# Kernel optimization log

Hardware: AMD Instinct MI355X
Metric: run time of the kernel (lower is better)

## Reference

```python
import jax, jax.numpy as jnp
import numpy as np

B, S, D, H = 2, 2048, 1024, 16
HD = D // H  # head_dim = 64
LN_EPS = 1e-5


def setup_inputs() -> dict:
    key = jax.random.key(0)
    ks = jax.random.split(key, 14)
    w = 0.02  # weight init scale
    return {
        "q": jax.random.normal(ks[0], (B, S, D), jnp.float32),
        "k": jax.random.normal(ks[1], (B, S, D), jnp.float32),
        "v": jax.random.normal(ks[2], (B, S, D), jnp.float32),
        "mask": jnp.zeros((B, 1, S, S), dtype=bool),
        "training": 0,
        "wq_w": jax.random.normal(ks[3], (D, D), jnp.float32) * w,
        "wq_b": jnp.zeros((D,), jnp.float32),
        "wk_w": jax.random.normal(ks[4], (D, D), jnp.float32) * w,
        "wk_b": jnp.zeros((D,), jnp.float32),
        "wv_w": jax.random.normal(ks[5], (D, D), jnp.float32) * w,
        "wv_b": jnp.zeros((D,), jnp.float32),
        "wo_w": jax.random.normal(ks[6], (D, D), jnp.float32) * w,
        "wo_b": jnp.zeros((D,), jnp.float32),
        "ln_g": jnp.ones((D,), jnp.float32),
        "ln_b": jnp.zeros((D,), jnp.float32),
    }


def _linear(x, w, b):
    # torch nn.Linear: x @ W.T + b, W is [out, in]
    return jnp.einsum('bsd,od->bso', x, w) + b


def _split_heads(x):
    b, s, _ = x.shape
    return x.reshape(b, s, H, HD).transpose(0, 2, 1, 3)  # [B,H,S,HD]


def reference(q, k, v, mask, training, wq_w, wq_b, wk_w, wk_b, wv_w, wv_b,
              wo_w, wo_b, ln_g, ln_b):
    residual = q
    Q = _split_heads(_linear(q, wq_w, wq_b))
    K = _split_heads(_linear(k, wk_w, wk_b))
    V = _split_heads(_linear(v, wv_w, wv_b))
    # source computes sqrt(dk) in float16, then adds 1e-8
    dk = jnp.sqrt(jnp.asarray(HD, jnp.float16)).astype(jnp.float32) + 1e-8
    score = jnp.einsum('bhqd,bhkd->bhqk', Q, K) / dk  # [B,H,S,S]
    # NOTE: source applies NO softmax; masked score is used directly.
    attn = jnp.where(mask, -jnp.inf, score)
    ctx = jnp.einsum('bhqk,bhkd->bhqd', attn, V)  # [B,H,S,HD]
    b, _, s, _ = ctx.shape
    ctx = ctx.transpose(0, 2, 1, 3).reshape(b, s, D)  # [B,S,D]
    o = _linear(ctx, wo_w, wo_b)
    # dropout is identity in eval mode
    x = residual + o
    mu = jnp.mean(x, axis=-1, keepdims=True)
    var = jnp.mean(jnp.square(x - mu), axis=-1, keepdims=True)
    return ln_g * (x - mu) * jax.lax.rsqrt(var + LN_EPS) + ln_b
```

## Files before the change

### kernel.cpp

```cpp
#include <hip/hip_runtime.h>


typedef __bf16 bf16;
typedef __bf16 bf16x8 __attribute__((ext_vector_type(8)));
typedef float f32x4 __attribute__((ext_vector_type(4)));

#define MFMA16(a, b, c) __builtin_amdgcn_mfma_f32_16x16x32_bf16(a, b, c, 0, 0, 0)
#define BARRIER() asm volatile("s_barrier" ::: "memory")
#define VMCNT4() asm volatile("s_waitcnt vmcnt(4)" ::: "memory")
#define VMCNT0() asm volatile("s_waitcnt vmcnt(0)" ::: "memory")
#define LGKM0()                                        \
  do {                                                 \
    asm volatile("s_waitcnt lgkmcnt(0)" ::: "memory"); \
    __builtin_amdgcn_sched_barrier(0);                 \
  } while (0)

__device__ __forceinline__ bf16x8 ld8(const bf16* p) { return *(const bf16x8*)p; }

__device__ __forceinline__ void gload16(const void* g, void* l) {
  __builtin_amdgcn_global_load_lds((__attribute__((address_space(1))) void*)(g),
                                   (__attribute__((address_space(3))) void*)(l), 16, 0, 0);
}

__device__ __forceinline__ int swz4(int row) { return (row ^ (row >> 2)) & 3; }

__device__ __forceinline__ bf16x8 cvt8(f32x4 lo, f32x4 hi) {
  bf16x8 o;
  o[0] = (bf16)lo[0]; o[1] = (bf16)lo[1]; o[2] = (bf16)lo[2]; o[3] = (bf16)lo[3];
  o[4] = (bf16)hi[0]; o[5] = (bf16)hi[1]; o[6] = (bf16)hi[2]; o[7] = (bf16)hi[3];
  return o;
}

__device__ __forceinline__ void compute16(const char* buf, const int aoff[4], const int boff[4],
                                          f32x4 (&acc)[4][4]) {
  bf16x8 av[4], bv[4];
#pragma unroll
  for (int i = 0; i < 4; i++) av[i] = *(const bf16x8*)(buf + aoff[i]);
#pragma unroll
  for (int j = 0; j < 4; j++) bv[j] = *(const bf16x8*)(buf + boff[j]);
  __builtin_amdgcn_s_setprio(1);
#pragma unroll
  for (int i = 0; i < 4; i++)
#pragma unroll
    for (int j = 0; j < 4; j++) acc[i][j] = MFMA16(av[i], bv[j], acc[i][j]);
  __builtin_amdgcn_s_setprio(0);
}

__device__ __forceinline__ void ring128(const bf16* __restrict__ A, const bf16* __restrict__ B,
                                        char* lds, f32x4 (&acc)[4][4]) {
  const int t = threadIdx.x;
  const int lane = t & 63, wid = t >> 6;
  const int wr = wid >> 1, wc = wid & 1;
  const int r16 = lane & 15, kg = lane >> 4;

  int aoff[4], boff[4];
#pragma unroll
  for (int i = 0; i < 4; i++) {
    int row = wr * 64 + i * 16 + r16;
    aoff[i] = row * 64 + ((kg ^ swz4(row)) << 4);
    row = wc * 64 + i * 16 + r16;
    boff[i] = 8192 + row * 64 + ((kg ^ swz4(row)) << 4);
  }

  const int r1 = t >> 2, c = t & 3, r2 = r1 + 64;
  const bf16* pa1 = A + (size_t)r1 * 1024 + (c ^ swz4(r1)) * 8;
  const bf16* pa2 = A + (size_t)r2 * 1024 + (c ^ swz4(r2)) * 8;
  const bf16* pb1 = B + (size_t)r1 * 1024 + (c ^ swz4(r1)) * 8;
  const bf16* pb2 = B + (size_t)r2 * 1024 + (c ^ swz4(r2)) * 8;
  const int d1 = wid << 10, d2 = 4096 + (wid << 10);

#pragma unroll
  for (int p = 0; p < 2; p++) {
    char* d = lds + p * 16384;
    gload16(pa1 + p * 32, d + d1);
    gload16(pa2 + p * 32, d + d2);
    gload16(pb1 + p * 32, d + 8192 + d1);
    gload16(pb2 + p * 32, d + 8192 + d2);
  }
  pa1 += 64; pa2 += 64; pb1 += 64; pb2 += 64;

  int cb = 0, rb = 2;
  for (int kt = 0; kt < 30; kt++) {
    VMCNT4();
    BARRIER();
    {
      char* d = lds + rb * 16384;
      gload16(pa1, d + d1);
      gload16(pa2, d + d2);
      gload16(pb1, d + 8192 + d1);
      gload16(pb2, d + 8192 + d2);
      pa1 += 32; pa2 += 32; pb1 += 32; pb2 += 32;
    }
    compute16(lds + cb * 16384, aoff, boff, acc);
    LGKM0();
    cb = (cb == 2) ? 0 : cb + 1;
    rb = (rb == 2) ? 0 : rb + 1;
  }
  VMCNT4(); BARRIER();
  compute16(lds + cb * 16384, aoff, boff, acc);
  LGKM0();
  cb = (cb == 2) ? 0 : cb + 1;
  VMCNT0(); BARRIER();
  compute16(lds + cb * 16384, aoff, boff, acc);
}

__device__ __forceinline__ void proj_epi(f32x4 (&acc)[4][4], const float* bias,
                                         bf16* __restrict__ C, int m0, int n0) {
  const int lane = threadIdx.x & 63, wid = threadIdx.x >> 6;
  const int wr = wid >> 1, wc = wid & 1, r16 = lane & 15, kg = lane >> 4;
#pragma unroll
  for (int j = 0; j < 4; j++) {
    const int col = n0 + wc * 64 + j * 16 + r16;
    const float bj = bias[col];
#pragma unroll
    for (int i = 0; i < 4; i++) {
      const int row = m0 + wr * 64 + i * 16 + kg * 4;
#pragma unroll
      for (int r = 0; r < 4; r++)
        C[(size_t)(row + r) * 1024 + col] = (bf16)(acc[i][j][r] + bj);
    }
  }
}

__global__ __launch_bounds__(256) void cvt_q_kernel(
    const float* __restrict__ q, const float* __restrict__ wq,
    bf16* __restrict__ q_bf, bf16* __restrict__ wq_bf, float* __restrict__ Mz) {
  const int bid = blockIdx.x;
  if (bid >= 2560) {
    float* p = Mz + (size_t)(bid - 2560) * 2048 + threadIdx.x * 8;
    *(f32x4*)p = f32x4{0.f, 0.f, 0.f, 0.f};
    *(f32x4*)(p + 4) = f32x4{0.f, 0.f, 0.f, 0.f};
    return;
  }
  const float* s; bf16* d; int x;
  if (bid < 2048) { s = q; d = q_bf; x = bid; }
  else            { s = wq; d = wq_bf; x = bid - 2048; }
  const size_t i = ((size_t)x * 256 + threadIdx.x) * 8;
  *(bf16x8*)(d + i) = cvt8(*(const f32x4*)(s + i), *(const f32x4*)(s + i + 4));
}

__global__ __launch_bounds__(256, 3) void fat1_kernel(
    const bf16* __restrict__ q_bf, const bf16* __restrict__ wq_bf,
    const float* __restrict__ bq, bf16* __restrict__ Q_bf,
    const float* __restrict__ k, const float* __restrict__ v,
    const float* __restrict__ wk, const float* __restrict__ wv,
    bf16* __restrict__ kv_bf, bf16* __restrict__ wkv_bf) {
  __shared__ __align__(1024) char lds[49152];
  const int wg = blockIdx.x;
  if (wg < 256) {
    const int swz = (wg & 7) * 32 + (wg >> 3);
    const int mt = swz >> 3, nt = swz & 7;
    const int m0 = mt * 128, n0 = nt * 128;
    f32x4 acc[4][4] = {};
    ring128(q_bf + (size_t)m0 * 1024, wq_bf + (size_t)n0 * 1024, lds, acc);
    proj_epi(acc, bq, Q_bf, m0, n0);
    return;
  }
  const int idx = wg - 256;
  const float* s; bf16* d; size_t dof; int x;
  if (idx < 4096) {
    const int y = idx >> 11; x = idx & 2047;
    s = (y == 0) ? k : v;
    d = kv_bf; dof = (size_t)y * 4194304u;
  } else {
    const int y = (idx - 4096) >> 9; x = (idx - 4096) & 511;
    s = (y == 0) ? wk : wv;
    d = wkv_bf; dof = (size_t)y * 1048576u;
  }
  const size_t i = ((size_t)x * 256 + threadIdx.x) * 8;
  *(bf16x8*)(d + dof + i) = cvt8(*(const f32x4*)(s + i), *(const f32x4*)(s + i + 4));
}

__global__ __launch_bounds__(256, 3) void gemm_proj_kv(
    const bf16* __restrict__ kv_bf, const bf16* __restrict__ wkv_bf,
    const float* __restrict__ bk, const float* __restrict__ bv,
    bf16* __restrict__ KV_out) {
  __shared__ __align__(1024) char lds[49152];
  const int wg = blockIdx.x;
  const int swz = (wg & 7) * 64 + (wg >> 3);
  const int mt = swz >> 3, nt = swz & 7;
  const int m0 = mt * 128, n0 = nt * 128;
  const int z = mt >> 5;

  f32x4 acc[4][4] = {};
  ring128(kv_bf + (size_t)m0 * 1024, wkv_bf + (size_t)z * 1048576u + (size_t)n0 * 1024, lds, acc);
  proj_epi(acc, z == 0 ? bk : bv, KV_out, m0, n0);
}

__global__ __launch_bounds__(256) void ktv_kernel(
    const bf16* __restrict__ Kb, const bf16* __restrict__ Vb, float* __restrict__ M) {
  const int bh = blockIdx.x >> 3, sc = blockIdx.x & 7;
  const int b = bh >> 4, h = bh & 15;
  __shared__ bf16 Kl[64][136];
  __shared__ bf16 Vl[64][136];
  const int t = threadIdx.x;
  const int l = t & 63, w = t >> 6;
  const int r16 = l & 15, kg = l >> 4;
  f32x4 acc[4] = {};
  for (int sub = 0; sub < 2; ++sub) {
    const int s0 = sc * 256 + sub * 128;
    const size_t base = ((size_t)b * 2048 + s0) * 1024 + h * 64;
    if (sub) __syncthreads();
#pragma unroll
    for (int p = 0; p < 4; p++) {
      const int chunk = p * 256 + t;
      const int s = chunk >> 3, d0 = (chunk & 7) * 8;
      bf16x8 kv = ld8(Kb + base + (size_t)s * 1024 + d0);
      bf16x8 vv = ld8(Vb + base + (size_t)s * 1024 + d0);
#pragma unroll
      for (int e = 0; e < 8; e++) { Kl[d0 + e][s] = kv[e]; Vl[d0 + e][s] = vv[e]; }
    }
    __syncthreads();
#pragma unroll
    for (int ks = 0; ks < 4; ks++) {
      bf16x8 a = ld8(&Kl[w * 16 + r16][ks * 32 + kg * 8]);
#pragma unroll
      for (int j = 0; j < 4; j++) {
        bf16x8 bvv = ld8(&Vl[j * 16 + r16][ks * 32 + kg * 8]);
        acc[j] = MFMA16(a, bvv, acc[j]);
      }
    }
  }
  float* Mh = M + (size_t)bh * 4096;
#pragma unroll
  for (int j = 0; j < 4; j++)
#pragma unroll
    for (int r = 0; r < 4; r++)
      atomicAdd(&Mh[(w * 16 + kg * 4 + r) * 64 + j * 16 + r16], acc[j][r]);
}

__global__ __launch_bounds__(256) void gt_kernel(
    const float* __restrict__ Wo, const float* __restrict__ M, bf16* __restrict__ Gt) {
  const int bid = blockIdx.x;
  const int b = bid >> 7, h = (bid >> 3) & 15, nt = bid & 7;
  const int n0 = nt * 128;
  const float* Mh = M + (size_t)((b << 4) + h) * 4096;
  const int l = threadIdx.x & 63, w = threadIdx.x >> 6;
  const int r16 = l & 15, kg = l >> 4;
  f32x4 acc[2][4] = {};
#pragma unroll
  for (int kk = 0; kk < 2; kk++) {
    bf16x8 a[2];
#pragma unroll
    for (int i = 0; i < 2; i++) {
      const float* wp = Wo + (size_t)(n0 + w * 32 + i * 16 + r16) * 1024 + h * 64 + kk * 32 + kg * 8;
      a[i] = cvt8(*(const f32x4*)wp, *(const f32x4*)(wp + 4));
    }
#pragma unroll
    for (int j = 0; j < 4; j++) {
      const float* mp = Mh + (j * 16 + r16) * 64 + kk * 32 + kg * 8;
      f32x4 m0v = *(const f32x4*)mp;
      f32x4 m1v = *(const f32x4*)(mp + 4);
      f32x4 sl = {m0v[0] * 0.125f, m0v[1] * 0.125f, m0v[2] * 0.125f, m0v[3] * 0.125f};
      f32x4 sh = {m1v[0] * 0.125f, m1v[1] * 0.125f, m1v[2] * 0.125f, m1v[3] * 0.125f};
      bf16x8 bv = cvt8(sl, sh);
#pragma unroll
      for (int i = 0; i < 2; i++) acc[i][j] = MFMA16(a[i], bv, acc[i][j]);
    }
  }
  bf16* G = Gt + (size_t)b * 1048576u;
#pragma unroll
  for (int i = 0; i < 2; i++)
#pragma unroll
    for (int j = 0; j < 4; j++)
#pragma unroll
      for (int r = 0; r < 4; r++)
        G[(size_t)(n0 + w * 32 + i * 16 + kg * 4 + r) * 1024 + h * 64 + j * 16 + r16] =
            (bf16)acc[i][j][r];
}

__global__ __launch_bounds__(256, 3) void gemm_out_r(
    const bf16* __restrict__ Q, const bf16* __restrict__ Gt,
    const float* __restrict__ bo, const float* __restrict__ resid, bf16* __restrict__ xb) {
  __shared__ __align__(1024) char lds[49152];
  const int wg = blockIdx.x;
  const int swz = (wg & 7) * 32 + (wg >> 3);
  const int mt = swz >> 3, nt = swz & 7;
  const int m0 = mt * 128, n0 = nt * 128;

  f32x4 acc[4][4] = {};
  ring128(Q + (size_t)m0 * 1024, Gt + (size_t)(m0 >> 11) * 1048576u + (size_t)n0 * 1024, lds, acc);

  const int lane = threadIdx.x & 63, wid = threadIdx.x >> 6;
  const int wr = wid >> 1, wc = wid & 1, r16 = lane & 15, kg = lane >> 4;
#pragma unroll
  for (int j = 0; j < 4; j++) {
    const int col = n0 + wc * 64 + j * 16 + r16;
    const float bj = bo[col];
#pragma unroll
    for (int i = 0; i < 4; i++) {
      const int row = m0 + wr * 64 + i * 16 + kg * 4;
#pragma unroll
      for (int r = 0; r < 4; r++) {
        const size_t off = (size_t)(row + r) * 1024 + col;
        xb[off] = (bf16)(acc[i][j][r] + bj + resid[off]);
      }
    }
  }
}

__global__ __launch_bounds__(256) void ln_kernel(
    const bf16* __restrict__ xb, const float* __restrict__ g, const float* __restrict__ bb,
    float* __restrict__ out) {
  const int lane = threadIdx.x & 63, wid = threadIdx.x >> 6;
  const int row = (blockIdx.x << 2) + wid;
  const bf16* xr = xb + (size_t)row * 1024;
  bf16x8 h0 = ld8(xr + lane * 16);
  bf16x8 h1 = ld8(xr + lane * 16 + 8);
  float v[16];
#pragma unroll
  for (int e = 0; e < 8; e++) { v[e] = (float)h0[e]; v[8 + e] = (float)h1[e]; }
  float s = 0.f, s2 = 0.f;
#pragma unroll
  for (int e = 0; e < 16; e++) { s += v[e]; s2 += v[e] * v[e]; }
#pragma unroll
  for (int m = 32; m; m >>= 1) { s += __shfl_xor(s, m); s2 += __shfl_xor(s2, m); }
  const float mu = s * (1.0f / 1024.0f);
  const float rstd = rsqrtf(s2 * (1.0f / 1024.0f) - mu * mu + 1e-5f);
  float* orow = out + (size_t)row * 1024 + lane * 16;
#pragma unroll
  for (int e = 0; e < 4; e++) {
    f32x4 gg = *(const f32x4*)(g + lane * 16 + e * 4);
    f32x4 bv = *(const f32x4*)(bb + lane * 16 + e * 4);
    f32x4 o;
#pragma unroll
    for (int u = 0; u < 4; u++) o[u] = gg[u] * ((v[e * 4 + u] - mu) * rstd) + bv[u];
    *(f32x4*)(orow + e * 4) = o;
  }
}

extern "C" void kernel_launch(void* const* d_in, const int* in_sizes, int n_in,
                              void* d_out, int out_size, void* d_ws, size_t ws_size,
                              hipStream_t stream) {
  (void)in_sizes; (void)n_in; (void)out_size; (void)ws_size;
  const float* q    = (const float*)d_in[0];
  const float* k    = (const float*)d_in[1];
  const float* v    = (const float*)d_in[2];
  const float* wq_w = (const float*)d_in[5];
  const float* wq_b = (const float*)d_in[6];
  const float* wk_w = (const float*)d_in[7];
  const float* wk_b = (const float*)d_in[8];
  const float* wv_w = (const float*)d_in[9];
  const float* wv_b = (const float*)d_in[10];
  const float* wo_w = (const float*)d_in[11];
  const float* wo_b = (const float*)d_in[12];
  const float* ln_g = (const float*)d_in[13];
  const float* ln_b = (const float*)d_in[14];
  float* out = (float*)d_out;

  bf16* wsb    = (bf16*)d_ws;
  bf16* q_bf   = wsb;
  bf16* kv_bf  = wsb + 4194304u;
  bf16* w_bf   = wsb + 12582912u;
  bf16* QKV_bf = wsb + 15728640u;
  float* M     = (float*)(wsb + 28311552u);
  bf16* Gt     = wsb;
  bf16* xb     = wsb + 2097152u;

  cvt_q_kernel<<<2624, 256, 0, stream>>>(q, wq_w, q_bf, w_bf, M);
  fat1_kernel<<<5376, 256, 0, stream>>>(q_bf, w_bf, wq_b, QKV_bf,
                                        k, v, wk_w, wv_w, kv_bf, w_bf + 1048576u);
  gemm_proj_kv<<<512, 256, 0, stream>>>(kv_bf, w_bf + 1048576u, wk_b, wv_b,
                                        QKV_bf + 4194304u);
  ktv_kernel<<<256, 256, 0, stream>>>(QKV_bf + 4194304u, QKV_bf + 8388608u, M);
  gt_kernel<<<256, 256, 0, stream>>>(wo_w, M, Gt);
  gemm_out_r<<<256, 256, 0, stream>>>(QKV_bf, Gt, wo_b, q, xb);
  ln_kernel<<<1024, 256, 0, stream>>>(xb, ln_g, ln_b, out);
}
```

Before: 92.05 us.

## Reschedule stages so K/V projection runs first and overlaps Q work

Reorders the pipeline. The K/V/weight conversion now runs first. The K/V projection GEMM runs in the same launch as the Q conversion. The Q projection GEMM shares a launch with the K^T V reduction, which reuses the GEMM's LDS buffer. This drops one kernel launch and lets independent memory-bound and compute-bound work overlap inside fused launches. The risk is load imbalance between the heterogeneous blocks and LDS/occupancy limits imposed on the ktv part by the 48KB allocation.

```diff
diff --git a/kernel.cpp b/kernel.cpp
--- a/kernel.cpp
+++ b/kernel.cpp
@@ -122,29 +122,61 @@
   }
 }
 
-__global__ __launch_bounds__(256) void cvt_q_kernel(
-    const float* __restrict__ q, const float* __restrict__ wq,
-    bf16* __restrict__ q_bf, bf16* __restrict__ wq_bf, float* __restrict__ Mz) {
+__global__ __launch_bounds__(256) void cvt_kvw_kernel(
+    const float* __restrict__ k, const float* __restrict__ v,
+    const float* __restrict__ wk, const float* __restrict__ wv,
+    bf16* __restrict__ kv_bf, bf16* __restrict__ wkv_bf, float* __restrict__ Mz) {
   const int bid = blockIdx.x;
-  if (bid >= 2560) {
-    float* p = Mz + (size_t)(bid - 2560) * 2048 + threadIdx.x * 8;
+  if (bid >= 5120) {
+    float* p = Mz + (size_t)(bid - 5120) * 2048 + threadIdx.x * 8;
     *(f32x4*)p = f32x4{0.f, 0.f, 0.f, 0.f};
     *(f32x4*)(p + 4) = f32x4{0.f, 0.f, 0.f, 0.f};
     return;
   }
+  const float* s; bf16* d; size_t dof; int x;
+  if (bid < 4096) {
+    const int y = bid >> 11; x = bid & 2047;
+    s = (y == 0) ? k : v;
+    d = kv_bf; dof = (size_t)y * 4194304u;
+  } else {
+    const int idx = bid - 4096; const int y = idx >> 9; x = idx & 511;
+    s = (y == 0) ? wk : wv;
+    d = wkv_bf; dof = (size_t)y * 1048576u;
+  }
+  const size_t i = ((size_t)x * 256 + threadIdx.x) * 8;
+  *(bf16x8*)(d + dof + i) = cvt8(*(const f32x4*)(s + i), *(const f32x4*)(s + i + 4));
+}
+
+__global__ __launch_bounds__(256, 3) void fat_a_kernel(
+    const bf16* __restrict__ kv_bf, const bf16* __restrict__ wkv_bf,
+    const float* __restrict__ bk, const float* __restrict__ bv, bf16* __restrict__ KV_out,
+    const float* __restrict__ q, const float* __restrict__ wq,
+    bf16* __restrict__ q_bf, bf16* __restrict__ wq_bf) {
+  __shared__ __align__(1024) char lds[49152];
+  const int wg = blockIdx.x;
+  if (wg < 512) {
+    const int swz = (wg & 7) * 64 + (wg >> 3);
+    const int mt = swz >> 3, nt = swz & 7;
+    const int m0 = mt * 128, n0 = nt * 128;
+    const int z = mt >> 5;
+    f32x4 acc[4][4] = {};
+    ring128(kv_bf + (size_t)m0 * 1024, wkv_bf + (size_t)z * 1048576u + (size_t)n0 * 1024,
+            lds, acc);
+    proj_epi(acc, z == 0 ? bk : bv, KV_out, m0, n0);
+    return;
+  }
+  const int idx = wg - 512;
   const float* s; bf16* d; int x;
-  if (bid < 2048) { s = q; d = q_bf; x = bid; }
-  else            { s = wq; d = wq_bf; x = bid - 2048; }
+  if (idx < 2048) { s = q; d = q_bf; x = idx; }
+  else            { s = wq; d = wq_bf; x = idx - 2048; }
   const size_t i = ((size_t)x * 256 + threadIdx.x) * 8;
   *(bf16x8*)(d + i) = cvt8(*(const f32x4*)(s + i), *(const f32x4*)(s + i + 4));
 }
 
-__global__ __launch_bounds__(256, 3) void fat1_kernel(
+__global__ __launch_bounds__(256, 3) void fat_b_kernel(
     const bf16* __restrict__ q_bf, const bf16* __restrict__ wq_bf,
     const float* __restrict__ bq, bf16* __restrict__ Q_bf,
-    const float* __restrict__ k, const float* __restrict__ v,
-    const float* __restrict__ wk, const float* __restrict__ wv,
-    bf16* __restrict__ kv_bf, bf16* __restrict__ wkv_bf) {
+    const bf16* __restrict__ Kb, const bf16* __restrict__ Vb, float* __restrict__ M) {
   __shared__ __align__(1024) char lds[49152];
   const int wg = blockIdx.x;
   if (wg < 256) {
@@ -156,43 +188,11 @@
     proj_epi(acc, bq, Q_bf, m0, n0);
     return;
   }
-  const int idx = wg - 256;
-  const float* s; bf16* d; size_t dof; int x;
-  if (idx < 4096) {
-    const int y = idx >> 11; x = idx & 2047;
-    s = (y == 0) ? k : v;
-    d = kv_bf; dof = (size_t)y * 4194304u;
-  } else {
-    const int y = (idx - 4096) >> 9; x = (idx - 4096) & 511;
-    s = (y == 0) ? wk : wv;
-    d = wkv_bf; dof = (size_t)y * 1048576u;
-  }
-  const size_t i = ((size_t)x * 256 + threadIdx.x) * 8;
-  *(bf16x8*)(d + dof + i) = cvt8(*(const f32x4*)(s + i), *(const f32x4*)(s + i + 4));
-}
-
-__global__ __launch_bounds__(256, 3) void gemm_proj_kv(
-    const bf16* __restrict__ kv_bf, const bf16* __restrict__ wkv_bf,
-    const float* __restrict__ bk, const float* __restrict__ bv,
-    bf16* __restrict__ KV_out) {
-  __shared__ __align__(1024) char lds[49152];
-  const int wg = blockIdx.x;
-  const int swz = (wg & 7) * 64 + (wg >> 3);
-  const int mt = swz >> 3, nt = swz & 7;
-  const int m0 = mt * 128, n0 = nt * 128;
-  const int z = mt >> 5;
-
-  f32x4 acc[4][4] = {};
-  ring128(kv_bf + (size_t)m0 * 1024, wkv_bf + (size_t)z * 1048576u + (size_t)n0 * 1024, lds, acc);
-  proj_epi(acc, z == 0 ? bk : bv, KV_out, m0, n0);
-}
-
-__global__ __launch_bounds__(256) void ktv_kernel(
-    const bf16* __restrict__ Kb, const bf16* __restrict__ Vb, float* __restrict__ M) {
-  const int bh = blockIdx.x >> 3, sc = blockIdx.x & 7;
+  bf16 (*Kl)[136] = (bf16(*)[136])lds;
+  bf16 (*Vl)[136] = (bf16(*)[136])(lds + 17408);
+  const int bid = wg - 256;
+  const int bh = bid >> 3, sc = bid & 7;
   const int b = bh >> 4, h = bh & 15;
-  __shared__ bf16 Kl[64][136];
-  __shared__ bf16 Vl[64][136];
   const int t = threadIdx.x;
   const int l = t & 63, w = t >> 6;
   const int r16 = l & 15, kg = l >> 4;
@@ -357,12 +357,11 @@
   bf16* Gt     = wsb;
   bf16* xb     = wsb + 2097152u;
 
-  cvt_q_kernel<<<2624, 256, 0, stream>>>(q, wq_w, q_bf, w_bf, M);
-  fat1_kernel<<<5376, 256, 0, stream>>>(q_bf, w_bf, wq_b, QKV_bf,
-                                        k, v, wk_w, wv_w, kv_bf, w_bf + 1048576u);
-  gemm_proj_kv<<<512, 256, 0, stream>>>(kv_bf, w_bf + 1048576u, wk_b, wv_b,
-                                        QKV_bf + 4194304u);
-  ktv_kernel<<<256, 256, 0, stream>>>(QKV_bf + 4194304u, QKV_bf + 8388608u, M);
+  cvt_kvw_kernel<<<5184, 256, 0, stream>>>(k, v, wk_w, wv_w, kv_bf, w_bf + 1048576u, M);
+  fat_a_kernel<<<3072, 256, 0, stream>>>(kv_bf, w_bf + 1048576u, wk_b, wv_b,
+                                         QKV_bf + 4194304u, q, wq_w, q_bf, w_bf);
+  fat_b_kernel<<<512, 256, 0, stream>>>(q_bf, w_bf, wq_b, QKV_bf,
+                                        QKV_bf + 4194304u, QKV_bf + 8388608u, M);
   gt_kernel<<<256, 256, 0, stream>>>(wo_w, M, Gt);
   gemm_out_r<<<256, 256, 0, stream>>>(QKV_bf, Gt, wo_b, q, xb);
   ln_kernel<<<1024, 256, 0, stream>>>(xb, ln_g, ln_b, out);
```

New measurement: 90.95 us. Within noise of the previous version (-1.2%).
